# Kernel optimization log

Measured on AMD Instinct MI355X. Metric: run time of the kernel, lower is better.

## Reference

```python
import jax, jax.numpy as jnp
import numpy as np
import math

D = 768
H = 8
DK = D // H
FF = 1024
EPS = 1e-5


def _layer_norm(x, g, b):
    m = jnp.mean(x, axis=-1, keepdims=True)
    v = jnp.mean((x - m) ** 2, axis=-1, keepdims=True)
    return (x - m) * jax.lax.rsqrt(v + EPS) * g + b


def _mha(x, attention_mask, Wq, bq, Wv, bv, g, b):
    # x: (B,S,D); attention_mask: (B,S,1) bool (True = masked/padding query row)
    B, S, _ = x.shape
    q = (x @ Wq + bq).reshape(B, S, H, DK).transpose(0, 2, 1, 3)  # (B,H,S,dk)
    # NOTE: original code uses the V projection for BOTH k and v (k = self.V(x))
    kv = (x @ Wv + bv).reshape(B, S, H, DK).transpose(0, 2, 1, 3)
    k = kv
    v = kv
    w = jnp.einsum('bhqd,bhkd->bhqk', q, k) / math.sqrt(DK)  # (B,H,S,S)
    pad = attention_mask[:, None, :, :]                      # (B,1,S,1) -> bcast (B,1,S,S)
    causal = jnp.triu(jnp.ones((S, S), dtype=bool), k=1)     # look-ahead mask
    mask = pad | causal
    w = jnp.where(mask, jnp.float32(-1e9), w)
    # NOTE: original uses nn.Softmax(dim=2) -> softmax over the QUERY axis
    score = jax.nn.softmax(w, axis=2)
    o = jnp.einsum('bhqk,bhkd->bhqd', score, v)              # (B,H,S,dk)
    o = o.transpose(0, 2, 1, 3).reshape(B, S, D)
    return _layer_norm(o + x, g, b)


def _ffn(x, W1, b1, W2, b2, g, b):
    h = jax.nn.relu(x @ W1 + b1)
    return _layer_norm(h @ W2 + b2 + x, g, b)


def setup_inputs() -> dict:
    key = jax.random.key(0)
    ks = jax.random.split(key, 16)
    B, S = 8, 1024
    sc = 0.02
    inp = {
        'x': jax.random.normal(ks[0], (B, S, D), dtype=jnp.float32),
        'attention_mask': jax.random.randint(ks[1], (B, S, 1), 0, 2).astype(bool),
    }
    for i, pre in enumerate(['a1', 'a2']):
        inp[pre + '_Wq'] = jax.random.normal(ks[2 + 4 * i], (D, D), dtype=jnp.float32) * sc
        inp[pre + '_bq'] = jnp.zeros((D,), dtype=jnp.float32)
        inp[pre + '_Wv'] = jax.random.normal(ks[3 + 4 * i], (D, D), dtype=jnp.float32) * sc
        inp[pre + '_bv'] = jnp.zeros((D,), dtype=jnp.float32)
        inp[pre + '_g'] = jnp.ones((D,), dtype=jnp.float32)
        inp[pre + '_b'] = jnp.zeros((D,), dtype=jnp.float32)
    inp['f_W1'] = jax.random.normal(ks[10], (D, FF), dtype=jnp.float32) * sc
    inp['f_b1'] = jnp.zeros((FF,), dtype=jnp.float32)
    inp['f_W2'] = jax.random.normal(ks[11], (FF, D), dtype=jnp.float32) * sc
    inp['f_b2'] = jnp.zeros((D,), dtype=jnp.float32)
    inp['f_g'] = jnp.ones((D,), dtype=jnp.float32)
    inp['f_b'] = jnp.zeros((D,), dtype=jnp.float32)
    return inp


def reference(x, attention_mask,
              a1_Wq, a1_bq, a1_Wv, a1_bv, a1_g, a1_b,
              a2_Wq, a2_bq, a2_Wv, a2_bv, a2_g, a2_b,
              f_W1, f_b1, f_W2, f_b2, f_g, f_b):
    x = _mha(x, attention_mask, a1_Wq, a1_bq, a1_Wv, a1_bv, a1_g, a1_b)
    x = _mha(x, attention_mask, a2_Wq, a2_bq, a2_Wv, a2_bv, a2_g, a2_b)
    x = _ffn(x, f_W1, f_b1, f_W2, f_b2, f_g, f_b)
    return x
```

## Files before the change

### kernel.cpp

```cpp
#include <hip/hip_runtime.h>
#include <cstddef>

#define BB 8
#define SS 1024
#define DD 768
#define HH 8
#define DKK 96
#define FFF 1024
#define MM (BB*SS)
#define QVW 1536
#define SM_SCALE 0.10206207261596577f
#define NTILES 16
#define NPAIR  136

typedef unsigned short ushort_t;
typedef short short8 __attribute__((ext_vector_type(8)));
typedef float f32x4 __attribute__((ext_vector_type(4)));
typedef ushort_t us4 __attribute__((ext_vector_type(4)));

__device__ __forceinline__ ushort_t f2b(float f) {
    union { float f; unsigned u; } x; x.f = f;
    unsigned r = x.u + 0x7fffu + ((x.u >> 16) & 1u);
    return (ushort_t)(r >> 16);
}
__device__ __forceinline__ float b2f(ushort_t u) {
    union { unsigned u; float f; } x; x.u = ((unsigned)u) << 16;
    return x.f;
}
__device__ __forceinline__ void gload16(const ushort_t* g, void* lds_base) {
    __builtin_amdgcn_global_load_lds(
        (const __attribute__((address_space(1))) unsigned int*)g,
        (__attribute__((address_space(3))) unsigned int*)lds_base, 16, 0, 0);
}

__global__ __launch_bounds__(256) void castWT(
    const float* __restrict__ W, ushort_t* __restrict__ Wt, int K, int N)
{
    __shared__ float T[32][33];
    const int tx = threadIdx.x & 31, ty = threadIdx.x >> 5;
    const int n0 = blockIdx.x * 32, k0 = blockIdx.y * 32;
    #pragma unroll
    for (int r = 0; r < 4; ++r)
        T[ty + 8*r][tx] = W[(size_t)(k0 + ty + 8*r) * N + n0 + tx];
    __syncthreads();
    #pragma unroll
    for (int r = 0; r < 4; ++r)
        Wt[(size_t)(n0 + ty + 8*r) * K + k0 + tx] = f2b(T[tx][ty + 8*r]);
}

__global__ __launch_bounds__(256) void castWT4(
    const float* __restrict__ Wa, const float* __restrict__ Wb,
    const float* __restrict__ Wc, const float* __restrict__ Wd,
    ushort_t* __restrict__ Ta, ushort_t* __restrict__ Tb,
    ushort_t* __restrict__ Tc, ushort_t* __restrict__ Td)
{
    __shared__ float T[32][33];
    const float* W; ushort_t* Wt;
    switch (blockIdx.z) {
        case 0:  W = Wa; Wt = Ta; break;
        case 1:  W = Wb; Wt = Tb; break;
        case 2:  W = Wc; Wt = Tc; break;
        default: W = Wd; Wt = Td; break;
    }
    const int tx = threadIdx.x & 31, ty = threadIdx.x >> 5;
    const int n0 = blockIdx.x * 32, k0 = blockIdx.y * 32;
    #pragma unroll
    for (int r = 0; r < 4; ++r)
        T[ty + 8*r][tx] = W[(size_t)(k0 + ty + 8*r) * DD + n0 + tx];
    __syncthreads();
    #pragma unroll
    for (int r = 0; r < 4; ++r)
        Wt[(size_t)(n0 + ty + 8*r) * DD + k0 + tx] = f2b(T[tx][ty + 8*r]);
}

__global__ __launch_bounds__(256) void cast_f2b(
    const float* __restrict__ in, ushort_t* __restrict__ out, int n4)
{
    const int i = blockIdx.x * 256 + threadIdx.x;
    if (i >= n4) return;
    const float4 v = ((const float4*)in)[i];
    us4 o; o.x = f2b(v.x); o.y = f2b(v.y); o.z = f2b(v.z); o.w = f2b(v.w);
    ((us4*)out)[i] = o;
}

template<int OUT_BF16, int RELU>
__global__ __launch_bounds__(256) void gemm_bt(
    const ushort_t* __restrict__ A, const ushort_t* __restrict__ Bt,
    const float* __restrict__ bias, const float* __restrict__ bias2, int bN,
    void* __restrict__ C, int K, int N)
{
    __shared__ ushort_t As[128*64];
    __shared__ ushort_t Bs[128*64];
    const int tid  = threadIdx.x;
    const int lane = tid & 63, wave = tid >> 6;
    const int wm = wave >> 1, wn = wave & 1;
    const int n = lane & 15, quad = lane >> 4;
    const int sx = n & 7;
    const int bm = blockIdx.y * 128, bn = blockIdx.x * 128;

    f32x4 acc[4][4];
    #pragma unroll
    for (int i = 0; i < 4; ++i)
        #pragma unroll
        for (int j = 0; j < 4; ++j) acc[i][j] = (f32x4){0.f, 0.f, 0.f, 0.f};

    for (int k0 = 0; k0 < K; k0 += 64) {
        #pragma unroll
        for (int it = 0; it < 4; ++it) {
            const int u   = (it*4 + wave)*64 + lane;
            const int row = u >> 3;
            const int c   = (u & 7) ^ (row & 7);
            gload16(A  + (size_t)(bm + row) * K + k0 + c*8, (char*)As + (it*4 + wave)*1024);
            gload16(Bt + (size_t)(bn + row) * K + k0 + c*8, (char*)Bs + (it*4 + wave)*1024);
        }
        __syncthreads();
        #pragma unroll
        for (int ks = 0; ks < 2; ++ks) {
            short8 af[4], bf[4];
            #pragma unroll
            for (int i = 0; i < 4; ++i)
                af[i] = *(short8*)&As[((wm*64 + i*16 + n)*8 + ((ks*4 + quad) ^ sx))*8];
            #pragma unroll
            for (int j = 0; j < 4; ++j)
                bf[j] = *(short8*)&Bs[((wn*64 + j*16 + n)*8 + ((ks*4 + quad) ^ sx))*8];
            #pragma unroll
            for (int i = 0; i < 4; ++i)
                #pragma unroll
                for (int j = 0; j < 4; ++j)
                    acc[i][j] = __builtin_amdgcn_mfma_f32_16x16x32_bf16(af[i], bf[j], acc[i][j], 0, 0, 0);
        }
        __syncthreads();
    }
    #pragma unroll
    for (int j = 0; j < 4; ++j) {
        const int col = bn + wn*64 + j*16 + n;
        const float bsv = (col < bN) ? bias[col] : bias2[col - bN];
        #pragma unroll
        for (int i = 0; i < 4; ++i) {
            const int row = bm + wm*64 + i*16 + quad*4;
            #pragma unroll
            for (int r = 0; r < 4; ++r) {
                float v = acc[i][j][r] + bsv;
                if (RELU) v = fmaxf(v, 0.f);
                if (OUT_BF16) ((ushort_t*)C)[(size_t)(row + r) * N + col] = f2b(v);
                else          ((float*)C)[(size_t)(row + r) * N + col]    = v;
            }
        }
    }
}

__global__ __launch_bounds__(256) void attn_scores(
    const ushort_t* __restrict__ QV, const int* __restrict__ amask,
    ushort_t* __restrict__ E, float* __restrict__ lpart)
{
    __shared__ ushort_t Qs[64*128];
    __shared__ ushort_t Ks[64*128];
    __shared__ float colsum[4][64];
    __shared__ float padf[64];
    const int tid = threadIdx.x, lane = tid & 63, wave = tid >> 6;
    const int n = lane & 15, quad = lane >> 4;
    const int sx = n & 7;
    const int t = blockIdx.x;
    int qt = (int)((-1.f + sqrtf(1.f + 8.f*(float)t)) * 0.5f);
    if ((qt+1)*(qt+2)/2 <= t) ++qt;
    if (qt*(qt+1)/2 > t) --qt;
    const int kt = t - qt*(qt+1)/2;
    const int q0 = qt*64, k0 = kt*64;
    const int h = blockIdx.y, b = blockIdx.z;
    const ushort_t* Qh = QV + (size_t)b*SS*QVW + h*DKK;
    const ushort_t* Kh = QV + (size_t)b*SS*QVW + DD + h*DKK;

    #pragma unroll
    for (int it = 0; it < 4; ++it) {
        const int u = (it*4 + wave)*64 + lane;
        const int row = u >> 4;
        const int c = (u & 15) ^ (row & 7);
        if (c < 12) {
            gload16(Qh + (size_t)(q0 + row)*QVW + c*8, (char*)Qs + (it*4 + wave)*1024);
            gload16(Kh + (size_t)(k0 + row)*QVW + c*8, (char*)Ks + (it*4 + wave)*1024);
        }
    }
    if (tid < 64) padf[tid] = (amask[b*SS + q0 + tid] != 0) ? 1.f : 0.f;
    __syncthreads();

    ushort_t* Et = E + (size_t)(b*HH + h)*NPAIR*4096 + (size_t)(qt*(qt+1)/2 + kt)*4096;

    #pragma unroll
    for (int ns = 0; ns < 4; ++ns) {
        f32x4 sa = (f32x4){0.f, 0.f, 0.f, 0.f};
        #pragma unroll
        for (int ks = 0; ks < 3; ++ks) {
            const short8 aq = *(short8*)&Qs[((wave*16 + n)*16 + ((ks*4 + quad) ^ sx))*8];
            const short8 bk = *(short8*)&Ks[((ns*16   + n)*16 + ((ks*4 + quad) ^ sx))*8];
            sa = __builtin_amdgcn_mfma_f32_16x16x32_bf16(aq, bk, sa, 0, 0, 0);
        }
        const int kl = ns*16 + n;
        const int keyg = k0 + kl;
        float s = 0.f;
        #pragma unroll
        for (int r = 0; r < 4; ++r) {
            const int qrow = wave*16 + quad*4 + r;
            const bool dead = (padf[qrow] != 0.f) || (keyg > q0 + qrow);
            const float e = dead ? 0.f : __expf(sa[r] * SM_SCALE);
            s += e;
            Et[qrow * 64 + kl] = f2b(e);
        }
        s += __shfl_xor(s, 16);
        s += __shfl_xor(s, 32);
        if (quad == 0) colsum[wave][kl] = s;
    }
    __syncthreads();
    if (tid < 64) {
        const float s = colsum[0][tid] + colsum[1][tid] + colsum[2][tid] + colsum[3][tid];
        lpart[((size_t)(b*HH + h)*NTILES + qt)*SS + k0 + tid] = s;
    }
}

__global__ __launch_bounds__(256) void transpose_scale(
    const ushort_t* __restrict__ QV, const float* __restrict__ lpart,
    ushort_t* __restrict__ Vt)
{
    __shared__ ushort_t T[64][104];
    __shared__ float rlv[64];
    const int tid = threadIdx.x;
    const int k0 = blockIdx.x * 64, h = blockIdx.y, b = blockIdx.z;
    const ushort_t* src = QV + (size_t)b*SS*QVW + DD + h*DKK;
    for (int s = tid; s < 768; s += 256) {
        const int r = s / 12, c = s % 12;
        *(short8*)&T[r][c*8] = *(const short8*)(src + (size_t)(k0 + r)*QVW + c*8);
    }
    if (tid < 64) {
        const float* lp = lpart + (size_t)(b*HH + h)*NTILES*SS;
        float l = 0.f;
        for (int qt = k0 >> 6; qt < NTILES; ++qt) l += lp[(size_t)qt*SS + k0 + tid];
        rlv[tid] = (l > 0.f) ? (1.f / l) : 0.f;
    }
    __syncthreads();
    ushort_t* dst = Vt + ((size_t)b*HH + h)*DKK*SS;
    for (int s = tid; s < 768; s += 256) {
        const int dk = s >> 3, c = s & 7;
        short8 v;
        #pragma unroll
        for (int i = 0; i < 8; ++i)
            v[i] = (short)f2b(b2f(T[c*8 + i][dk]) * rlv[c*8 + i]);
        *(short8*)(dst + (size_t)dk*SS + k0 + c*8) = v;
    }
}

__global__ __launch_bounds__(256) void attn_pv(
    const ushort_t* __restrict__ E, const ushort_t* __restrict__ Vt,
    float* __restrict__ O)
{
    __shared__ ushort_t Es[64*64];
    __shared__ ushort_t Vs[96*64];
    const int tid = threadIdx.x, lane = tid & 63, wave = tid >> 6;
    const int n = lane & 15, quad = lane >> 4;
    const int sx = n & 7;
    const int px = blockIdx.x;
    const int h = blockIdx.y, b = blockIdx.z;
    const ushort_t* Eb  = E + (size_t)(b*HH + h)*NPAIR*4096;
    const ushort_t* Vth = Vt + ((size_t)b*HH + h)*DKK*SS;

    #pragma unroll
    for (int half = 0; half < 2; ++half) {
        const int qt = half ? (15 - px) : px;
        const int q0 = qt * 64;
        f32x4 acc[6];
        #pragma unroll
        for (int t = 0; t < 6; ++t) acc[t] = (f32x4){0.f, 0.f, 0.f, 0.f};
        const ushort_t* Eq = Eb + (size_t)(qt*(qt+1)/2)*4096;

        for (int kt = 0; kt <= qt; ++kt) {
            const ushort_t* Et = Eq + (size_t)kt*4096;
            #pragma unroll
            for (int it = 0; it < 2; ++it) {
                const int u = (it*4 + wave)*64 + lane;
                const int row = u >> 3, c = (u & 7) ^ (row & 7);
                gload16(Et + (size_t)row*64 + c*8, (char*)Es + (it*4 + wave)*1024);
            }
            #pragma unroll
            for (int it = 0; it < 3; ++it) {
                const int u = (it*4 + wave)*64 + lane;
                const int row = u >> 3, c = (u & 7) ^ (row & 7);
                gload16(Vth + (size_t)row*SS + kt*64 + c*8, (char*)Vs + (it*4 + wave)*1024);
            }
            __syncthreads();
            #pragma unroll
            for (int kk = 0; kk < 2; ++kk) {
                const short8 ae = *(short8*)&Es[((wave*16 + n)*8 + ((kk*4 + quad) ^ sx))*8];
                #pragma unroll
                for (int nt = 0; nt < 6; ++nt) {
                    const short8 bv = *(short8*)&Vs[((nt*16 + n)*8 + ((kk*4 + quad) ^ sx))*8];
                    acc[nt] = __builtin_amdgcn_mfma_f32_16x16x32_bf16(ae, bv, acc[nt], 0, 0, 0);
                }
            }
            __syncthreads();
        }
        #pragma unroll
        for (int nt = 0; nt < 6; ++nt) {
            #pragma unroll
            for (int r = 0; r < 4; ++r) {
                const int q = q0 + wave*16 + quad*4 + r;
                O[((size_t)b*SS + q)*DD + h*DKK + nt*16 + n] = acc[nt][r];
            }
        }
    }
}

__device__ __forceinline__ float block_sum256(float s, float* tmp4)
{
    #pragma unroll
    for (int off = 32; off > 0; off >>= 1) s += __shfl_down(s, off);
    __syncthreads();
    if ((threadIdx.x & 63) == 0) tmp4[threadIdx.x >> 6] = s;
    __syncthreads();
    return tmp4[0] + tmp4[1] + tmp4[2] + tmp4[3];
}

__global__ __launch_bounds__(256) void resid_ln(
    const float* __restrict__ X, const float* __restrict__ R,
    const float* __restrict__ g, const float* __restrict__ beta,
    float* __restrict__ Out, ushort_t* __restrict__ OutB)
{
    __shared__ float tmp4[4];
    const int row = blockIdx.x;
    const int tid = threadIdx.x;
    const float* xp = X + (size_t)row * DD;
    const float* rp = R + (size_t)row * DD;
    float v[3], s = 0.f;
    #pragma unroll
    for (int i = 0; i < 3; ++i) {
        v[i] = xp[tid + 256*i] + rp[tid + 256*i];
        s += v[i];
    }
    const float mu = block_sum256(s, tmp4) * (1.f / DD);
    float qv = 0.f;
    #pragma unroll
    for (int i = 0; i < 3; ++i) { const float d = v[i] - mu; qv += d * d; }
    const float inv = rsqrtf(block_sum256(qv, tmp4) * (1.f / DD) + 1e-5f);
    #pragma unroll
    for (int i = 0; i < 3; ++i) {
        const int c = tid + 256*i;
        const float o = (v[i] - mu) * inv * g[c] + beta[c];
        Out[(size_t)row * DD + c] = o;
        if (OutB) OutB[(size_t)row * DD + c] = f2b(o);
    }
}

extern "C" void kernel_launch(void* const* d_in, const int* in_sizes, int n_in,
                              void* d_out, int out_size, void* d_ws, size_t ws_size,
                              hipStream_t stream)
{
    (void)in_sizes; (void)n_in; (void)out_size; (void)ws_size;
    const float* x0    = (const float*)d_in[0];
    const int*   amask = (const int*)d_in[1];
    const float* a1_Wq = (const float*)d_in[2];
    const float* a1_bq = (const float*)d_in[3];
    const float* a1_Wv = (const float*)d_in[4];
    const float* a1_bv = (const float*)d_in[5];
    const float* a1_g  = (const float*)d_in[6];
    const float* a1_b  = (const float*)d_in[7];
    const float* a2_Wq = (const float*)d_in[8];
    const float* a2_bq = (const float*)d_in[9];
    const float* a2_Wv = (const float*)d_in[10];
    const float* a2_bv = (const float*)d_in[11];
    const float* a2_g  = (const float*)d_in[12];
    const float* a2_b  = (const float*)d_in[13];
    const float* f_W1  = (const float*)d_in[14];
    const float* f_b1  = (const float*)d_in[15];
    const float* f_W2  = (const float*)d_in[16];
    const float* f_b2  = (const float*)d_in[17];
    const float* f_g   = (const float*)d_in[18];
    const float* f_b   = (const float*)d_in[19];

    char* ws = (char*)d_ws;
    size_t off = 0;
    auto alloc = [&](size_t bytes) { void* p = ws + off; off += (bytes + 255) & ~(size_t)255; return p; };
    ushort_t* WqvT1 = (ushort_t*)alloc((size_t)QVW*DD*2);
    ushort_t* WqvT2 = (ushort_t*)alloc((size_t)QVW*DD*2);
    ushort_t* W1T   = (ushort_t*)alloc((size_t)DD*FFF*2);
    ushort_t* W2T   = (ushort_t*)alloc((size_t)DD*FFF*2);
    ushort_t* xb    = (ushort_t*)alloc((size_t)MM*DD*2);
    ushort_t* QVb   = (ushort_t*)alloc((size_t)MM*QVW*2);
    ushort_t* hb    = QVb;
    ushort_t* Vtb   = (ushort_t*)alloc((size_t)MM*DD*2);
    float* t0    = (float*)alloc((size_t)MM*DD*4);
    float* lpart = (float*)alloc((size_t)BB*HH*NTILES*SS*4);
    ushort_t* Ebuf = (ushort_t*)alloc((size_t)BB*HH*NPAIR*4096*2);
    float* out = (float*)d_out;

    const dim3 blk(256);
    const dim3 gsc(NPAIR, HH, BB);
    const dim3 gpv(NTILES/2, HH, BB);
    const dim3 gtr(SS/64, HH, BB);
    const dim3 gqv(QVW/128, MM/128);
    const dim3 gf1(FFF/128, MM/128);
    const dim3 gf2(DD/128, MM/128);

    castWT4<<<dim3(DD/32, DD/32, 4), blk, 0, stream>>>(
        a1_Wq, a1_Wv, a2_Wq, a2_Wv,
        WqvT1, WqvT1 + (size_t)DD*DD, WqvT2, WqvT2 + (size_t)DD*DD);
    castWT<<<dim3(FFF/32, DD/32), blk, 0, stream>>>(f_W1, W1T, DD, FFF);
    castWT<<<dim3(DD/32, FFF/32), blk, 0, stream>>>(f_W2, W2T, FFF, DD);
    cast_f2b<<<(MM*DD/4 + 255)/256, blk, 0, stream>>>(x0, xb, MM*DD/4);

    gemm_bt<1,0><<<gqv, blk, 0, stream>>>(xb, WqvT1, a1_bq, a1_bv, DD, QVb, DD, QVW);
    attn_scores<<<gsc, blk, 0, stream>>>(QVb, amask, Ebuf, lpart);
    transpose_scale<<<gtr, blk, 0, stream>>>(QVb, lpart, Vtb);
    attn_pv<<<gpv, blk, 0, stream>>>(Ebuf, Vtb, t0);
    resid_ln<<<dim3(MM), blk, 0, stream>>>(t0, x0, a1_g, a1_b, t0, xb);

    gemm_bt<1,0><<<gqv, blk, 0, stream>>>(xb, WqvT2, a2_bq, a2_bv, DD, QVb, DD, QVW);
    attn_scores<<<gsc, blk, 0, stream>>>(QVb, amask, Ebuf, lpart);
    transpose_scale<<<gtr, blk, 0, stream>>>(QVb, lpart, Vtb);
    attn_pv<<<gpv, blk, 0, stream>>>(Ebuf, Vtb, out);
    resid_ln<<<dim3(MM), blk, 0, stream>>>(out, t0, a2_g, a2_b, out, xb);

    gemm_bt<1,1><<<gf1, blk, 0, stream>>>(xb, W1T, f_b1, f_b1, FFF, hb, DD, FFF);
    gemm_bt<0,0><<<gf2, blk, 0, stream>>>(hb, W2T, f_b2, f_b2, DD, t0, FFF, DD);
    resid_ln<<<dim3(MM), blk, 0, stream>>>(t0, out, f_g, f_b, out, (ushort_t*)nullptr);
}
```

Measured before the change: 441.7 us.

## Stage GEMM and score outputs through LDS and keep intermediate activations in bf16

The GEMM epilogue now writes bf16 results into a padded shared-memory tile and stores them to global memory as coalesced 16-byte vectors. The attention score tile is staged the same way. Attention output, residual inputs and the FFN second GEMM output are kept in bf16 instead of fp32, so the layer-norm kernels read bf16 and only the final one writes fp32. This cuts global memory traffic and uncoalesced scalar stores, at the cost of extra rounding in residual paths and more LDS use per block.

```diff
diff --git a/kernel.cpp b/kernel.cpp
--- a/kernel.cpp
+++ b/kernel.cpp
@@ -83,14 +83,15 @@
     ((us4*)out)[i] = o;
 }
 
-template<int OUT_BF16, int RELU>
+template<int RELU>
 __global__ __launch_bounds__(256) void gemm_bt(
     const ushort_t* __restrict__ A, const ushort_t* __restrict__ Bt,
     const float* __restrict__ bias, const float* __restrict__ bias2, int bN,
-    void* __restrict__ C, int K, int N)
-{
-    __shared__ ushort_t As[128*64];
-    __shared__ ushort_t Bs[128*64];
+    ushort_t* __restrict__ C, int K, int N)
+{
+    __shared__ ushort_t S[128*136];
+    ushort_t* As = S;
+    ushort_t* Bs = S + 128*64;
     const int tid  = threadIdx.x;
     const int lane = tid & 63, wave = tid >> 6;
     const int wm = wave >> 1, wn = wave & 1;
@@ -133,19 +134,26 @@
     }
     #pragma unroll
     for (int j = 0; j < 4; ++j) {
-        const int col = bn + wn*64 + j*16 + n;
-        const float bsv = (col < bN) ? bias[col] : bias2[col - bN];
+        const int col = wn*64 + j*16 + n;
+        const int gcol = bn + col;
+        const float bsv = (gcol < bN) ? bias[gcol] : bias2[gcol - bN];
         #pragma unroll
         for (int i = 0; i < 4; ++i) {
-            const int row = bm + wm*64 + i*16 + quad*4;
+            const int lrow = wm*64 + i*16 + quad*4;
             #pragma unroll
             for (int r = 0; r < 4; ++r) {
                 float v = acc[i][j][r] + bsv;
                 if (RELU) v = fmaxf(v, 0.f);
-                if (OUT_BF16) ((ushort_t*)C)[(size_t)(row + r) * N + col] = f2b(v);
-                else          ((float*)C)[(size_t)(row + r) * N + col]    = v;
+                S[(lrow + r)*136 + col] = f2b(v);
             }
         }
+    }
+    __syncthreads();
+    #pragma unroll
+    for (int it = 0; it < 8; ++it) {
+        const int u = it*256 + tid;
+        const int grow = u >> 4, gc = u & 15;
+        *(short8*)(C + (size_t)(bm + grow)*N + bn + gc*8) = *(short8*)&S[grow*136 + gc*8];
     }
 }
 
@@ -155,6 +163,7 @@
 {
     __shared__ ushort_t Qs[64*128];
     __shared__ ushort_t Ks[64*128];
+    __shared__ ushort_t Etile[64*72];
     __shared__ float colsum[4][64];
     __shared__ float padf[64];
     const int tid = threadIdx.x, lane = tid & 63, wave = tid >> 6;
@@ -203,13 +212,19 @@
             const bool dead = (padf[qrow] != 0.f) || (keyg > q0 + qrow);
             const float e = dead ? 0.f : __expf(sa[r] * SM_SCALE);
             s += e;
-            Et[qrow * 64 + kl] = f2b(e);
+            Etile[qrow*72 + kl] = f2b(e);
         }
         s += __shfl_xor(s, 16);
         s += __shfl_xor(s, 32);
         if (quad == 0) colsum[wave][kl] = s;
     }
     __syncthreads();
+    #pragma unroll
+    for (int it = 0; it < 2; ++it) {
+        const int u = it*256 + tid;
+        const int grow = u >> 3, gc = u & 7;
+        *(short8*)(Et + grow*64 + gc*8) = *(short8*)&Etile[grow*72 + gc*8];
+    }
     if (tid < 64) {
         const float s = colsum[0][tid] + colsum[1][tid] + colsum[2][tid] + colsum[3][tid];
         lpart[((size_t)(b*HH + h)*NTILES + qt)*SS + k0 + tid] = s;
@@ -249,7 +264,7 @@
 
 __global__ __launch_bounds__(256) void attn_pv(
     const ushort_t* __restrict__ E, const ushort_t* __restrict__ Vt,
-    float* __restrict__ O)
+    ushort_t* __restrict__ O)
 {
     __shared__ ushort_t Es[64*64];
     __shared__ ushort_t Vs[96*64];
@@ -301,7 +316,7 @@
             #pragma unroll
             for (int r = 0; r < 4; ++r) {
                 const int q = q0 + wave*16 + quad*4 + r;
-                O[((size_t)b*SS + q)*DD + h*DKK + nt*16 + n] = acc[nt][r];
+                O[((size_t)b*SS + q)*DD + h*DKK + nt*16 + n] = f2b(acc[nt][r]);
             }
         }
     }
@@ -317,20 +332,22 @@
     return tmp4[0] + tmp4[1] + tmp4[2] + tmp4[3];
 }
 
+template<int XBF, int RBF, int OUTF32>
 __global__ __launch_bounds__(256) void resid_ln(
-    const float* __restrict__ X, const float* __restrict__ R,
+    const void* __restrict__ X, const void* __restrict__ R,
     const float* __restrict__ g, const float* __restrict__ beta,
-    float* __restrict__ Out, ushort_t* __restrict__ OutB)
+    ushort_t* __restrict__ OutB, float* __restrict__ OutF)
 {
     __shared__ float tmp4[4];
     const int row = blockIdx.x;
     const int tid = threadIdx.x;
-    const float* xp = X + (size_t)row * DD;
-    const float* rp = R + (size_t)row * DD;
     float v[3], s = 0.f;
     #pragma unroll
     for (int i = 0; i < 3; ++i) {
-        v[i] = xp[tid + 256*i] + rp[tid + 256*i];
+        const size_t idx = (size_t)row * DD + tid + 256*i;
+        const float xv = XBF ? b2f(((const ushort_t*)X)[idx]) : ((const float*)X)[idx];
+        const float rv = RBF ? b2f(((const ushort_t*)R)[idx]) : ((const float*)R)[idx];
+        v[i] = xv + rv;
         s += v[i];
     }
     const float mu = block_sum256(s, tmp4) * (1.f / DD);
@@ -342,8 +359,8 @@
     for (int i = 0; i < 3; ++i) {
         const int c = tid + 256*i;
         const float o = (v[i] - mu) * inv * g[c] + beta[c];
-        Out[(size_t)row * DD + c] = o;
-        if (OutB) OutB[(size_t)row * DD + c] = f2b(o);
+        if (OUTF32) OutF[(size_t)row * DD + c] = o;
+        else        OutB[(size_t)row * DD + c] = f2b(o);
     }
 }
 
@@ -380,11 +397,13 @@
     ushort_t* WqvT2 = (ushort_t*)alloc((size_t)QVW*DD*2);
     ushort_t* W1T   = (ushort_t*)alloc((size_t)DD*FFF*2);
     ushort_t* W2T   = (ushort_t*)alloc((size_t)DD*FFF*2);
-    ushort_t* xb    = (ushort_t*)alloc((size_t)MM*DD*2);
+    ushort_t* xb0   = (ushort_t*)alloc((size_t)MM*DD*2);
+    ushort_t* xb1   = (ushort_t*)alloc((size_t)MM*DD*2);
+    ushort_t* xb2   = (ushort_t*)alloc((size_t)MM*DD*2);
+    ushort_t* Ob    = (ushort_t*)alloc((size_t)MM*DD*2);
     ushort_t* QVb   = (ushort_t*)alloc((size_t)MM*QVW*2);
     ushort_t* hb    = QVb;
     ushort_t* Vtb   = (ushort_t*)alloc((size_t)MM*DD*2);
-    float* t0    = (float*)alloc((size_t)MM*DD*4);
     float* lpart = (float*)alloc((size_t)BB*HH*NTILES*SS*4);
     ushort_t* Ebuf = (ushort_t*)alloc((size_t)BB*HH*NPAIR*4096*2);
     float* out = (float*)d_out;
@@ -402,21 +421,21 @@
         WqvT1, WqvT1 + (size_t)DD*DD, WqvT2, WqvT2 + (size_t)DD*DD);
     castWT<<<dim3(FFF/32, DD/32), blk, 0, stream>>>(f_W1, W1T, DD, FFF);
     castWT<<<dim3(DD/32, FFF/32), blk, 0, stream>>>(f_W2, W2T, FFF, DD);
-    cast_f2b<<<(MM*DD/4 + 255)/256, blk, 0, stream>>>(x0, xb, MM*DD/4);
-
-    gemm_bt<1,0><<<gqv, blk, 0, stream>>>(xb, WqvT1, a1_bq, a1_bv, DD, QVb, DD, QVW);
+    cast_f2b<<<(MM*DD/4 + 255)/256, blk, 0, stream>>>(x0, xb0, MM*DD/4);
+
+    gemm_bt<0><<<gqv, blk, 0, stream>>>(xb0, WqvT1, a1_bq, a1_bv, DD, QVb, DD, QVW);
     attn_scores<<<gsc, blk, 0, stream>>>(QVb, amask, Ebuf, lpart);
     transpose_scale<<<gtr, blk, 0, stream>>>(QVb, lpart, Vtb);
-    attn_pv<<<gpv, blk, 0, stream>>>(Ebuf, Vtb, t0);
-    resid_ln<<<dim3(MM), blk, 0, stream>>>(t0, x0, a1_g, a1_b, t0, xb);
-
-    gemm_bt<1,0><<<gqv, blk, 0, stream>>>(xb, WqvT2, a2_bq, a2_bv, DD, QVb, DD, QVW);
+    attn_pv<<<gpv, blk, 0, stream>>>(Ebuf, Vtb, Ob);
+    resid_ln<1,0,0><<<dim3(MM), blk, 0, stream>>>(Ob, x0, a1_g, a1_b, xb1, nullptr);
+
+    gemm_bt<0><<<gqv, blk, 0, stream>>>(xb1, WqvT2, a2_bq, a2_bv, DD, QVb, DD, QVW);
     attn_scores<<<gsc, blk, 0, stream>>>(QVb, amask, Ebuf, lpart);
     transpose_scale<<<gtr, blk, 0, stream>>>(QVb, lpart, Vtb);
-    attn_pv<<<gpv, blk, 0, stream>>>(Ebuf, Vtb, out);
-    resid_ln<<<dim3(MM), blk, 0, stream>>>(out, t0, a2_g, a2_b, out, xb);
-
-    gemm_bt<1,1><<<gf1, blk, 0, stream>>>(xb, W1T, f_b1, f_b1, FFF, hb, DD, FFF);
-    gemm_bt<0,0><<<gf2, blk, 0, stream>>>(hb, W2T, f_b2, f_b2, DD, t0, FFF, DD);
-    resid_ln<<<dim3(MM), blk, 0, stream>>>(t0, out, f_g, f_b, out, (ushort_t*)nullptr);
-}
+    attn_pv<<<gpv, blk, 0, stream>>>(Ebuf, Vtb, Ob);
+    resid_ln<1,1,0><<<dim3(MM), blk, 0, stream>>>(Ob, xb1, a2_g, a2_b, xb2, nullptr);
+
+    gemm_bt<1><<<gf1, blk, 0, stream>>>(xb2, W1T, f_b1, f_b1, FFF, hb, DD, FFF);
+    gemm_bt<0><<<gf2, blk, 0, stream>>>(hb, W2T, f_b2, f_b2, DD, Ob, FFF, DD);
+    resid_ln<1,1,1><<<dim3(MM), blk, 0, stream>>>(Ob, xb2, f_g, f_b, nullptr, out);
+}
```

Result: faster. 407.1 us (-7.8%).
